# Performance work log

Hardware: AMD Instinct MI355X
Metric: run time of the kernel (lower is better)

## Reference

```python
import jax, jax.numpy as jnp
import numpy as np

N_HEAD = 16


def setup_inputs() -> dict:
    key = jax.random.key(0)
    ks = jax.random.split(key, 6)
    B, T, C = 2, 2048, 1024
    x = jax.random.normal(ks[0], (B, T, C), dtype=jnp.float32)
    mask = jnp.ones((B, T), dtype=jnp.int32)
    s = 1.0 / np.sqrt(C)
    Wqkv = jax.random.normal(ks[1], (C, 3 * C), dtype=jnp.float32) * s
    bqkv = jax.random.normal(ks[2], (3 * C,), dtype=jnp.float32) * 0.02
    Wproj = jax.random.normal(ks[3], (C, C), dtype=jnp.float32) * s
    bproj = jax.random.normal(ks[4], (C,), dtype=jnp.float32) * 0.02
    return {"x": x, "mask": mask, "Wqkv": Wqkv, "bqkv": bqkv,
            "Wproj": Wproj, "bproj": bproj}


def reference(x, mask, Wqkv, bqkv, Wproj, bproj):
    B, T, C = x.shape
    H = N_HEAD
    Dh = C // H
    scale = 1.0 / np.sqrt(Dh)
    qkv = x @ Wqkv + bqkv                       # [B,T,3C]
    q, k, v = jnp.split(qkv, 3, axis=-1)
    # [B,T,C] -> [B,H,T,Dh]
    q = q.reshape(B, T, H, Dh).transpose(0, 2, 1, 3)
    k = k.reshape(B, T, H, Dh).transpose(0, 2, 1, 3)
    v = v.reshape(B, T, H, Dh).transpose(0, 2, 1, 3)
    attn = jnp.einsum('bhid,bhjd->bhij', q, k) * scale  # [B,H,T,T]
    m = mask[:, None, None, :]                  # b j -> b 1 1 j
    attn = jnp.where(m == 0, -jnp.inf, attn)
    attn = jax.nn.softmax(attn, axis=-1)
    y = jnp.einsum('bhij,bhjd->bhid', attn, v)  # [B,H,T,Dh]
    y = y.transpose(0, 2, 1, 3).reshape(B, T, C)
    return y @ Wproj + bproj
```

## Files before the change

kernel.cpp:

```cpp
#include <hip/hip_runtime.h>

using US   = unsigned short;
using bf8  = __attribute__((ext_vector_type(8))) __bf16;
using us8  = __attribute__((ext_vector_type(8))) US;
using us4  = __attribute__((ext_vector_type(4))) US;
using f4   = __attribute__((ext_vector_type(4))) float;
using f8   = __attribute__((ext_vector_type(8))) float;
using f16v = __attribute__((ext_vector_type(16))) float;
using i4   = __attribute__((ext_vector_type(4))) int;
using u2   = __attribute__((ext_vector_type(2))) unsigned;

__device__ __forceinline__ US f2bf(float x) {
  union { float f; unsigned u; } v; v.f = x;
  unsigned r = v.u + 0x7fffu + ((v.u >> 16) & 1u);
  return (US)(r >> 16);
}
__device__ __forceinline__ unsigned cvtpk(float a, float b) {
  unsigned r;
  asm("v_cvt_pk_bf16_f32 %0, %1, %2" : "=v"(r) : "v"(a), "v"(b));
  return r;
}
#if __has_builtin(__builtin_amdgcn_exp2f)
__device__ __forceinline__ float ex2(float x) { return __builtin_amdgcn_exp2f(x); }
#else
__device__ __forceinline__ float ex2(float x) {
  float r;
  asm("v_exp_f32 %0, %1" : "=v"(r) : "v"(x));
  return r;
}
#endif
__device__ __forceinline__ void gl16(const US* g, US* l) {
  __builtin_amdgcn_global_load_lds((const __attribute__((address_space(1))) void*)g,
                                   (__attribute__((address_space(3))) void*)l, 16, 0, 0);
}

__global__ void cvt_k(const float* __restrict__ in, US* __restrict__ out, int n8) {
  int i = blockIdx.x * blockDim.x + threadIdx.x;
  if (i >= n8) return;
  f8 v = ((const f8*)in)[i];
  us8 o;
#pragma unroll
  for (int j = 0; j < 8; ++j) o[j] = f2bf(v[j]);
  ((us8*)out)[i] = o;
}

__global__ void trw_k(const float* __restrict__ in, US* __restrict__ out, int R, int C) {
  __shared__ float tile[32][33];
  int bx = blockIdx.x * 32, by = blockIdx.y * 32;
  int tx = threadIdx.x & 31, ty = threadIdx.x >> 5;
  for (int i = ty; i < 32; i += 8)
    tile[i][tx] = in[(size_t)(by + i) * C + bx + tx];
  __syncthreads();
  for (int i = ty; i < 32; i += 8)
    out[(size_t)(bx + i) * R + by + tx] = f2bf(tile[tx][i]);
}

__device__ __forceinline__ int SW4(int row) { return (row & 3) ^ ((row >> 2) & 3); }

template <typename OT, bool QSC = false, bool VT = false>
__global__ __launch_bounds__(256, 2) void gemm_ct(const US* __restrict__ A,
                                                  const US* __restrict__ Bt,
                                                  const float* __restrict__ bias,
                                                  OT* __restrict__ out,
                                                  US* __restrict__ vtout,
                                                  int M, int N, int K) {
  __shared__ US lA[3][128 * 32];
  __shared__ US lB[3][128 * 32];
  const int t = threadIdx.x;
  const int lane = t & 63;
  const int w = t >> 6;
  const int wr = w >> 1, wc = w & 1;
  const int l15 = lane & 15, g = lane >> 4;
  const int m0 = blockIdx.x * 128, n0 = blockIdx.y * 128;

  float bv[4];
#pragma unroll
  for (int ni = 0; ni < 4; ++ni)
    bv[ni] = bias ? bias[n0 + wc * 64 + ni * 16 + l15] : 0.0f;

  const int r16 = lane >> 2;
  const int u4 = lane & 3;
  const int csw = (u4 ^ SW4(r16)) * 8;

#define GSTAGE(buf, k0s)                                                          \
  {                                                                               \
    _Pragma("unroll") for (int s = 0; s < 2; ++s) {                               \
      const int rb = w * 32 + s * 16;                                             \
      gl16(A + (size_t)(m0 + rb + r16) * K + (k0s) + csw, &lA[buf][rb * 32]);     \
      gl16(Bt + (size_t)(n0 + rb + r16) * K + (k0s) + csw, &lB[buf][rb * 32]);    \
    }                                                                             \
  }

  GSTAGE(0, 0);

  f4 acc[4][4] = {};
  const int kk = K >> 5;
  int cur = 0;
  for (int tt = 0; tt < kk; ++tt) {
    if (tt + 1 < kk) {
      int nb = cur + 1; if (nb == 3) nb = 0;
      GSTAGE(nb, (tt + 1) * 32);
      asm volatile("s_waitcnt vmcnt(4)" ::: "memory");
    } else {
      asm volatile("s_waitcnt vmcnt(0)" ::: "memory");
    }
    __builtin_amdgcn_s_barrier();
    asm volatile("" ::: "memory");

    const US* a_ = lA[cur];
    const US* b_ = lB[cur];
    bf8 af[4], bfr[4];
#pragma unroll
    for (int mi = 0; mi < 4; ++mi) {
      int row = wr * 64 + mi * 16 + l15;
      af[mi] = *(const bf8*)((const char*)a_ + row * 64 + ((g ^ SW4(row)) << 4));
    }
#pragma unroll
    for (int ni = 0; ni < 4; ++ni) {
      int row = wc * 64 + ni * 16 + l15;
      bfr[ni] = *(const bf8*)((const char*)b_ + row * 64 + ((g ^ SW4(row)) << 4));
    }
    __builtin_amdgcn_s_setprio(1);
#pragma unroll
    for (int mi = 0; mi < 4; ++mi)
#pragma unroll
      for (int ni = 0; ni < 4; ++ni)
        acc[mi][ni] = __builtin_amdgcn_mfma_f32_16x16x32_bf16(af[mi], bfr[ni], acc[mi][ni], 0, 0, 0);
    __builtin_amdgcn_s_setprio(0);
    cur = cur + 1 == 3 ? 0 : cur + 1;
  }
#undef GSTAGE

  if (VT && n0 >= 2048) {
#pragma unroll
    for (int ni = 0; ni < 4; ++ni) {
      int cv = n0 - 2048 + wc * 64 + ni * 16 + l15;
      int h2 = cv >> 6, d = cv & 63;
#pragma unroll
      for (int mi = 0; mi < 4; ++mi) {
        int rowb = m0 + wr * 64 + mi * 16 + g * 4;
        int bb = rowb >> 11, tloc = rowb & 2047;
        us4 pk;
#pragma unroll
        for (int r = 0; r < 4; ++r) pk[r] = f2bf(acc[mi][ni][r] + bv[ni]);
        *(us4*)(vtout + ((size_t)(bb * 16 + h2) * 64 + d) * 2048 + tloc) = pk;
      }
    }
    return;
  }
  const float oscale = (QSC && n0 < 1024) ? 0.18033688011f : 1.0f;
#pragma unroll
  for (int ni = 0; ni < 4; ++ni) {
    int col = n0 + wc * 64 + ni * 16 + l15;
#pragma unroll
    for (int mi = 0; mi < 4; ++mi) {
      int rowb = m0 + wr * 64 + mi * 16 + g * 4;
#pragma unroll
      for (int r = 0; r < 4; ++r) {
        float val = (acc[mi][ni][r] + bv[ni]) * oscale;
        if constexpr (sizeof(OT) == 2)
          out[(size_t)(rowb + r) * N + col] = f2bf(val);
        else
          out[(size_t)(rowb + r) * N + col] = val;
      }
    }
  }
}

__device__ __forceinline__ const bf8* fragp(const US* base, int r, int ks, int hi) {
  int byte = r * 128 + ((((ks << 1) | hi) ^ (r & 7)) << 4);
  return (const bf8*)((const char*)base + byte);
}

__global__ __launch_bounds__(256, 2) void attn_k(const US* __restrict__ qkv,
                                                 const US* __restrict__ vt,
                                                 const int* __restrict__ mask,
                                                 US* __restrict__ y) {
  int f0 = blockIdx.x;
  int f = ((f0 & 7) << 6) | (f0 >> 3);
  const int qt = f & 15;
  const int bh = f >> 4;
  const int b = bh >> 4;
  const int h = bh & 15;
  const int lane = threadIdx.x & 63, w = threadIdx.x >> 6;
  const int l31 = lane & 31, hi = lane >> 5;

  __shared__ US lK[3][64 * 64];
  __shared__ US lV[3][64 * 64];
  __shared__ unsigned char lMaskB[256];

  const int qr0 = qt * 128 + w * 32;
  const US* qrow = qkv + (size_t)(b * 2048 + qr0 + l31) * 3072 + h * 64 + hi * 8;
  bf8 qf[4];
#pragma unroll
  for (int ks = 0; ks < 4; ++ks) qf[ks] = *(const bf8*)(qrow + ks * 16);

  const int r8 = lane >> 3;
  const int c16 = (lane & 7) ^ r8;
  const US* kg = qkv + (size_t)b * 2048 * 3072 + 1024 + h * 64 + c16 * 8;
  const US* vg = vt + (size_t)bh * 64 * 2048 + c16 * 8;
  const int R0 = w * 16;

  f16v o0 = {}, o1 = {};
  f16v osum = {};
  bf8 ones;
  {
    union { US u[8]; bf8 v; } on;
#pragma unroll
    for (int i = 0; i < 8; ++i) on.u[i] = 0x3F80;
    ones = on.v;
  }

#define STAGE(buf, j0s)                                                        \
  {                                                                            \
    gl16(kg + (size_t)((j0s) + R0 + r8) * 3072, &lK[buf][R0 * 64]);            \
    gl16(kg + (size_t)((j0s) + R0 + 8 + r8) * 3072, &lK[buf][(R0 + 8) * 64]);  \
    gl16(vg + (size_t)(R0 + r8) * 2048 + (j0s), &lV[buf][R0 * 64]);            \
    gl16(vg + (size_t)(R0 + 8 + r8) * 2048 + (j0s), &lV[buf][(R0 + 8) * 64]);  \
  }

  STAGE(0, 0);

  int allones;
  {
    const int t8 = threadIdx.x * 8;
    i4 ma = *(const i4*)(mask + b * 2048 + t8);
    i4 mc = *(const i4*)(mask + b * 2048 + t8 + 4);
    unsigned byte = 0;
#pragma unroll
    for (int k = 0; k < 4; ++k) {
      byte |= (ma[k] != 0 ? 1u : 0u) << k;
      byte |= (mc[k] != 0 ? 1u : 0u) << (k + 4);
    }
    lMaskB[threadIdx.x] = (unsigned char)byte;
    allones = __syncthreads_and((int)(byte == 0xFFu));
  }

#define ATILE(tt, CUR, NXT, LAST)                                              \
  {                                                                            \
    const int j0_ = (tt) * 64;                                                 \
    if (!(LAST)) {                                                             \
      STAGE(NXT, j0_ + 64);                                                    \
      asm volatile("s_waitcnt vmcnt(4)" ::: "memory");                         \
    } else {                                                                   \
      asm volatile("s_waitcnt vmcnt(0)" ::: "memory");                         \
    }                                                                          \
    __builtin_amdgcn_s_barrier();                                              \
    asm volatile("" ::: "memory");                                             \
    const US* lKc = lK[CUR];                                                   \
    const US* lVc = lV[CUR];                                                   \
    f16v s0 = {}, s1 = {};                                                     \
    __builtin_amdgcn_s_setprio(1);                                             \
    _Pragma("unroll") for (int ks = 0; ks < 4; ++ks) {                         \
      bf8 ka0 = *fragp(lKc, l31, ks, hi);                                      \
      bf8 ka1 = *fragp(lKc, 32 + l31, ks, hi);                                 \
      s0 = __builtin_amdgcn_mfma_f32_32x32x16_bf16(ka0, qf[ks], s0, 0, 0, 0);  \
      s1 = __builtin_amdgcn_mfma_f32_32x32x16_bf16(ka1, qf[ks], s1, 0, 0, 0);  \
    }                                                                          \
    __builtin_amdgcn_s_setprio(0);                                             \
    _Pragma("unroll") for (int i = 0; i < 16; ++i) {                           \
      s0[i] = ex2(s0[i]);                                                      \
      s1[i] = ex2(s1[i]);                                                      \
    }                                                                          \
    if (!allones) {                                                            \
      unsigned mbyte = lMaskB[(j0_ >> 3) + (lane >> 3)];                       \
      int mword = (mbyte >> (lane & 7)) & 1;                                   \
      unsigned long long mbits = __ballot(mword != 0);                         \
      _Pragma("unroll") for (int i = 0; i < 16; ++i) {                         \
        int r = (i & 3) + 8 * (i >> 2) + 4 * hi;                               \
        if (!((mbits >> r) & 1)) s0[i] = 0.0f;                                 \
        if (!((mbits >> (32 + r)) & 1)) s1[i] = 0.0f;                          \
      }                                                                        \
    }                                                                          \
    bf8 pf[4];                                                                 \
    _Pragma("unroll") for (int ks = 0; ks < 4; ++ks) {                         \
      const f16v& st = (ks < 2) ? s0 : s1;                                     \
      const int R = (ks & 1) * 8;                                              \
      unsigned w0 = cvtpk(st[R + 0], st[R + 1]);                               \
      unsigned w1 = cvtpk(st[R + 2], st[R + 3]);                               \
      unsigned w2 = cvtpk(st[R + 4], st[R + 5]);                               \
      unsigned w3 = cvtpk(st[R + 6], st[R + 7]);                               \
      u2 p02 = __builtin_amdgcn_permlane32_swap(w0, w2, false, false);         \
      u2 p13 = __builtin_amdgcn_permlane32_swap(w1, w3, false, false);         \
      union { unsigned u[4]; bf8 v; } bld;                                     \
      bld.u[0] = p02[0];                                                       \
      bld.u[1] = p13[0];                                                       \
      bld.u[2] = p02[1];                                                       \
      bld.u[3] = p13[1];                                                       \
      pf[ks] = bld.v;                                                          \
    }                                                                          \
    __builtin_amdgcn_s_setprio(1);                                             \
    _Pragma("unroll") for (int ks = 0; ks < 4; ++ks) {                         \
      bf8 vf0 = *fragp(lVc, l31, ks, hi);                                      \
      bf8 vf1 = *fragp(lVc, 32 + l31, ks, hi);                                 \
      o0 = __builtin_amdgcn_mfma_f32_32x32x16_bf16(vf0, pf[ks], o0, 0, 0, 0);  \
      o1 = __builtin_amdgcn_mfma_f32_32x32x16_bf16(vf1, pf[ks], o1, 0, 0, 0);  \
      osum = __builtin_amdgcn_mfma_f32_32x32x16_bf16(ones, pf[ks], osum, 0, 0, 0); \
    }                                                                          \
    __builtin_amdgcn_s_setprio(0);                                             \
  }

  for (int gg = 0; gg < 10; ++gg) {
    const int t3 = gg * 3;
    ATILE(t3, 0, 1, 0)
    ATILE(t3 + 1, 1, 2, 0)
    ATILE(t3 + 2, 2, 0, 0)
  }
  ATILE(30, 0, 1, 0)
  ATILE(31, 1, 2, 1)
#undef ATILE
#undef STAGE

  float inv = 1.0f / osum[0];
  US* yrow = y + (size_t)(b * 2048 + qr0 + l31) * 1024 + h * 64;
#pragma unroll
  for (int qd = 0; qd < 4; ++qd) {
    us4 pk0, pk1;
#pragma unroll
    for (int j = 0; j < 4; ++j) {
      pk0[j] = f2bf(o0[qd * 4 + j] * inv);
      pk1[j] = f2bf(o1[qd * 4 + j] * inv);
    }
    *(us4*)(yrow + qd * 8 + hi * 4) = pk0;
    *(us4*)(yrow + 32 + qd * 8 + hi * 4) = pk1;
  }
}

extern "C" void kernel_launch(void* const* d_in, const int* in_sizes, int n_in,
                              void* d_out, int out_size, void* d_ws, size_t ws_size,
                              hipStream_t stream) {
  const float* x     = (const float*)d_in[0];
  const int*   mask  = (const int*)d_in[1];
  const float* Wqkv  = (const float*)d_in[2];
  const float* bqkv  = (const float*)d_in[3];
  const float* Wproj = (const float*)d_in[4];
  const float* bproj = (const float*)d_in[5];
  float* out = (float*)d_out;

  US* xb     = (US*)d_ws;
  US* qkvb   = xb     + (size_t)4096 * 1024;
  US* WqkvT  = qkvb   + (size_t)4096 * 3072;
  US* WprojT = WqkvT  + (size_t)3072 * 1024;
  US* Vt     = WprojT + (size_t)1024 * 1024;
  US* yb     = Vt     + (size_t)32 * 64 * 2048;

  cvt_k<<<2048, 256, 0, stream>>>(x, xb, 4096 * 1024 / 8);
  trw_k<<<dim3(96, 32), 256, 0, stream>>>(Wqkv, WqkvT, 1024, 3072);
  trw_k<<<dim3(32, 32), 256, 0, stream>>>(Wproj, WprojT, 1024, 1024);
  gemm_ct<US, true, true><<<dim3(32, 24), 256, 0, stream>>>(xb, WqkvT, bqkv, qkvb, Vt, 4096, 3072, 1024);
  attn_k<<<512, 256, 0, stream>>>(qkvb, Vt, mask, yb);
  gemm_ct<float><<<dim3(32, 8), 256, 0, stream>>>(yb, WprojT, bproj, out, nullptr, 4096, 1024, 1024);
}
```

Baseline: 117.6 us.

## Split attention KV range across waves within a block and merge partial outputs

The attention kernel now uses a 64-row query tile. Its four waves form a 2x2 grid: two query halves times two key halves, with each key half covering 1024 keys in 32-key tiles, and the grid doubles to 1024 blocks. Each KV-half wave pair stages its own K/V tiles into separate LDS buffers, and V uses a new 32-column swizzle. The partial numerators and denominators are combined through LDS at the end. The aim is more, smaller blocks for better load balance. The cost is a doubled K/V read volume per query, half the MFMA work between barriers, and an extra cross-wave reduction.

Result: slower. 126.4 us (+7.4%).

```diff
diff --git a/kernel.cpp b/kernel.cpp
--- a/kernel.cpp
+++ b/kernel.cpp
@@ -167,8 +167,12 @@
   }
 }
 
-__device__ __forceinline__ const bf8* fragp(const US* base, int r, int ks, int hi) {
-  int byte = r * 128 + ((((ks << 1) | hi) ^ (r & 7)) << 4);
+__device__ __forceinline__ const bf8* fragp(const US* base, int r, int u) {
+  int byte = r * 128 + ((u ^ (r & 7)) << 4);
+  return (const bf8*)((const char*)base + byte);
+}
+__device__ __forceinline__ const bf8* vfragp(const US* base, int r, int u) {
+  int byte = r * 64 + ((u ^ (r & 3)) << 4);
   return (const bf8*)((const char*)base + byte);
 }
 
@@ -177,19 +181,20 @@
                                                  const int* __restrict__ mask,
                                                  US* __restrict__ y) {
   int f0 = blockIdx.x;
-  int f = ((f0 & 7) << 6) | (f0 >> 3);
-  const int qt = f & 15;
-  const int bh = f >> 4;
+  int f = ((f0 & 7) << 7) | (f0 >> 3);
+  const int qt = f & 31;
+  const int bh = f >> 5;
   const int b = bh >> 4;
   const int h = bh & 15;
   const int lane = threadIdx.x & 63, w = threadIdx.x >> 6;
   const int l31 = lane & 31, hi = lane >> 5;
-
-  __shared__ US lK[3][64 * 64];
-  __shared__ US lV[3][64 * 64];
+  const int qh = w & 1, kh = w >> 1;
+
+  __shared__ US lK[2][3][32 * 64];
+  __shared__ US lV[2][3][64 * 32];
   __shared__ unsigned char lMaskB[256];
 
-  const int qr0 = qt * 128 + w * 32;
+  const int qr0 = qt * 64 + qh * 32;
   const US* qrow = qkv + (size_t)(b * 2048 + qr0 + l31) * 3072 + h * 64 + hi * 8;
   bf8 qf[4];
 #pragma unroll
@@ -198,8 +203,10 @@
   const int r8 = lane >> 3;
   const int c16 = (lane & 7) ^ r8;
   const US* kg = qkv + (size_t)b * 2048 * 3072 + 1024 + h * 64 + c16 * 8;
-  const US* vg = vt + (size_t)bh * 64 * 2048 + c16 * 8;
-  const int R0 = w * 16;
+  const int vr16 = lane >> 2;
+  const int vc4 = (lane & 3) ^ (vr16 & 3);
+  const US* vg = vt + (size_t)bh * 64 * 2048 + vc4 * 8;
+  const int kv0 = kh * 1024;
 
   f16v o0 = {}, o1 = {};
   f16v osum = {};
@@ -211,15 +218,15 @@
     ones = on.v;
   }
 
-#define STAGE(buf, j0s)                                                        \
-  {                                                                            \
-    gl16(kg + (size_t)((j0s) + R0 + r8) * 3072, &lK[buf][R0 * 64]);            \
-    gl16(kg + (size_t)((j0s) + R0 + 8 + r8) * 3072, &lK[buf][(R0 + 8) * 64]);  \
-    gl16(vg + (size_t)(R0 + r8) * 2048 + (j0s), &lV[buf][R0 * 64]);            \
-    gl16(vg + (size_t)(R0 + 8 + r8) * 2048 + (j0s), &lV[buf][(R0 + 8) * 64]);  \
-  }
-
-  STAGE(0, 0);
+#define STAGE(buf, j0s)                                                          \
+  {                                                                              \
+    gl16(kg + (size_t)((j0s) + qh * 16 + r8) * 3072, &lK[kh][buf][(qh * 16) * 64]); \
+    gl16(kg + (size_t)((j0s) + qh * 16 + 8 + r8) * 3072, &lK[kh][buf][(qh * 16 + 8) * 64]); \
+    gl16(vg + (size_t)(qh * 32 + vr16) * 2048 + (j0s), &lV[kh][buf][(qh * 32) * 32]); \
+    gl16(vg + (size_t)(qh * 32 + 16 + vr16) * 2048 + (j0s), &lV[kh][buf][(qh * 32 + 16) * 32]); \
+  }
+
+  STAGE(0, kv0);
 
   int allones;
   {
@@ -238,48 +245,39 @@
 
 #define ATILE(tt, CUR, NXT, LAST)                                              \
   {                                                                            \
-    const int j0_ = (tt) * 64;                                                 \
+    const int j0_ = kv0 + (tt) * 32;                                           \
     if (!(LAST)) {                                                             \
-      STAGE(NXT, j0_ + 64);                                                    \
+      STAGE(NXT, j0_ + 32);                                                    \
       asm volatile("s_waitcnt vmcnt(4)" ::: "memory");                         \
     } else {                                                                   \
       asm volatile("s_waitcnt vmcnt(0)" ::: "memory");                         \
     }                                                                          \
     __builtin_amdgcn_s_barrier();                                              \
     asm volatile("" ::: "memory");                                             \
-    const US* lKc = lK[CUR];                                                   \
-    const US* lVc = lV[CUR];                                                   \
-    f16v s0 = {}, s1 = {};                                                     \
+    const US* lKc = lK[kh][CUR];                                               \
+    const US* lVc = lV[kh][CUR];                                               \
+    f16v s0 = {};                                                              \
     __builtin_amdgcn_s_setprio(1);                                             \
     _Pragma("unroll") for (int ks = 0; ks < 4; ++ks) {                         \
-      bf8 ka0 = *fragp(lKc, l31, ks, hi);                                      \
-      bf8 ka1 = *fragp(lKc, 32 + l31, ks, hi);                                 \
+      bf8 ka0 = *fragp(lKc, l31, 2 * ks + hi);                                 \
       s0 = __builtin_amdgcn_mfma_f32_32x32x16_bf16(ka0, qf[ks], s0, 0, 0, 0);  \
-      s1 = __builtin_amdgcn_mfma_f32_32x32x16_bf16(ka1, qf[ks], s1, 0, 0, 0);  \
     }                                                                          \
     __builtin_amdgcn_s_setprio(0);                                             \
-    _Pragma("unroll") for (int i = 0; i < 16; ++i) {                           \
-      s0[i] = ex2(s0[i]);                                                      \
-      s1[i] = ex2(s1[i]);                                                      \
-    }                                                                          \
+    _Pragma("unroll") for (int i = 0; i < 16; ++i) s0[i] = ex2(s0[i]);         \
     if (!allones) {                                                            \
-      unsigned mbyte = lMaskB[(j0_ >> 3) + (lane >> 3)];                       \
-      int mword = (mbyte >> (lane & 7)) & 1;                                   \
-      unsigned long long mbits = __ballot(mword != 0);                         \
+      unsigned mbits = *(const unsigned*)&lMaskB[j0_ >> 3];                    \
       _Pragma("unroll") for (int i = 0; i < 16; ++i) {                         \
         int r = (i & 3) + 8 * (i >> 2) + 4 * hi;                               \
         if (!((mbits >> r) & 1)) s0[i] = 0.0f;                                 \
-        if (!((mbits >> (32 + r)) & 1)) s1[i] = 0.0f;                          \
       }                                                                        \
     }                                                                          \
-    bf8 pf[4];                                                                 \
-    _Pragma("unroll") for (int ks = 0; ks < 4; ++ks) {                         \
-      const f16v& st = (ks < 2) ? s0 : s1;                                     \
-      const int R = (ks & 1) * 8;                                              \
-      unsigned w0 = cvtpk(st[R + 0], st[R + 1]);                               \
-      unsigned w1 = cvtpk(st[R + 2], st[R + 3]);                               \
-      unsigned w2 = cvtpk(st[R + 4], st[R + 5]);                               \
-      unsigned w3 = cvtpk(st[R + 6], st[R + 7]);                               \
+    bf8 pf[2];                                                                 \
+    _Pragma("unroll") for (int ks = 0; ks < 2; ++ks) {                         \
+      const int R = ks * 8;                                                    \
+      unsigned w0 = cvtpk(s0[R + 0], s0[R + 1]);                               \
+      unsigned w1 = cvtpk(s0[R + 2], s0[R + 3]);                               \
+      unsigned w2 = cvtpk(s0[R + 4], s0[R + 5]);                               \
+      unsigned w3 = cvtpk(s0[R + 6], s0[R + 7]);                               \
       u2 p02 = __builtin_amdgcn_permlane32_swap(w0, w2, false, false);         \
       u2 p13 = __builtin_amdgcn_permlane32_swap(w1, w3, false, false);         \
       union { unsigned u[4]; bf8 v; } bld;                                     \
@@ -290,9 +288,9 @@
       pf[ks] = bld.v;                                                          \
     }                                                                          \
     __builtin_amdgcn_s_setprio(1);                                             \
-    _Pragma("unroll") for (int ks = 0; ks < 4; ++ks) {                         \
-      bf8 vf0 = *fragp(lVc, l31, ks, hi);                                      \
-      bf8 vf1 = *fragp(lVc, 32 + l31, ks, hi);                                 \
+    _Pragma("unroll") for (int ks = 0; ks < 2; ++ks) {                         \
+      bf8 vf0 = *vfragp(lVc, l31, 2 * ks + hi);                                \
+      bf8 vf1 = *vfragp(lVc, 32 + l31, 2 * ks + hi);                           \
       o0 = __builtin_amdgcn_mfma_f32_32x32x16_bf16(vf0, pf[ks], o0, 0, 0, 0);  \
       o1 = __builtin_amdgcn_mfma_f32_32x32x16_bf16(vf1, pf[ks], o1, 0, 0, 0);  \
       osum = __builtin_amdgcn_mfma_f32_32x32x16_bf16(ones, pf[ks], osum, 0, 0, 0); \
@@ -311,18 +309,32 @@
 #undef ATILE
 #undef STAGE
 
-  float inv = 1.0f / osum[0];
-  US* yrow = y + (size_t)(b * 2048 + qr0 + l31) * 1024 + h * 64;
-#pragma unroll
-  for (int qd = 0; qd < 4; ++qd) {
-    us4 pk0, pk1;
-#pragma unroll
-    for (int j = 0; j < 4; ++j) {
-      pk0[j] = f2bf(o0[qd * 4 + j] * inv);
-      pk1[j] = f2bf(o1[qd * 4 + j] * inv);
-    }
-    *(us4*)(yrow + qd * 8 + hi * 4) = pk0;
-    *(us4*)(yrow + 32 + qd * 8 + hi * 4) = pk1;
+  __syncthreads();
+  float* xch = (float*)&lK[0][0][0];
+  const int xi = (qh * 64 + lane) * 34;
+  if (kh) {
+#pragma unroll
+    for (int i = 0; i < 16; ++i) xch[xi + i] = o0[i];
+#pragma unroll
+    for (int i = 0; i < 16; ++i) xch[xi + 16 + i] = o1[i];
+    xch[xi + 32] = osum[0];
+  }
+  __syncthreads();
+  if (!kh) {
+    float inv = 1.0f / (osum[0] + xch[xi + 32]);
+    US* yrow = y + (size_t)(b * 2048 + qr0 + l31) * 1024 + h * 64;
+#pragma unroll
+    for (int qd = 0; qd < 4; ++qd) {
+      us4 pk0, pk1;
+#pragma unroll
+      for (int j = 0; j < 4; ++j) {
+        int i = qd * 4 + j;
+        pk0[j] = f2bf((o0[i] + xch[xi + i]) * inv);
+        pk1[j] = f2bf((o1[i] + xch[xi + 16 + i]) * inv);
+      }
+      *(us4*)(yrow + qd * 8 + hi * 4) = pk0;
+      *(us4*)(yrow + 32 + qd * 8 + hi * 4) = pk1;
+    }
   }
 }
 
@@ -348,6 +360,6 @@
   trw_k<<<dim3(96, 32), 256, 0, stream>>>(Wqkv, WqkvT, 1024, 3072);
   trw_k<<<dim3(32, 32), 256, 0, stream>>>(Wproj, WprojT, 1024, 1024);
   gemm_ct<US, true, true><<<dim3(32, 24), 256, 0, stream>>>(xb, WqkvT, bqkv, qkvb, Vt, 4096, 3072, 1024);
-  attn_k<<<512, 256, 0, stream>>>(qkvb, Vt, mask, yb);
+  attn_k<<<1024, 256, 0, stream>>>(qkvb, Vt, mask, yb);
   gemm_ct<float><<<dim3(32, 8), 256, 0, stream>>>(yb, WprojT, bproj, out, nullptr, 4096, 1024, 1024);
 }
```
